# Performance work log

Hardware: AMD Instinct MI355X
Metric: run time of the kernel (lower is better)

## Reference

```python
import jax, jax.numpy as jnp
import numpy as np


def _conv1x1(x, w, b):
    # x: [B,Cin,H,W], w: [Cout,Cin], b: [Cout]
    return jnp.einsum('bchw,oc->bohw', x, w) + b[None, :, None, None]


def setup_inputs() -> dict:
    key = jax.random.key(0)
    ks = jax.random.split(key, 9)
    C, Cb = 256, 128
    B, H, W = 8, 32, 32
    s_in = 1.0 / np.sqrt(C)
    s_bn = 1.0 / np.sqrt(Cb)
    return {
        'x': jax.random.normal(ks[0], (B, C, H, W), dtype=jnp.float32),
        'theta_w': jax.random.uniform(ks[1], (Cb, C), jnp.float32, -s_in, s_in),
        'theta_b': jax.random.uniform(ks[2], (Cb,), jnp.float32, -s_in, s_in),
        'phi_w': jax.random.uniform(ks[3], (Cb, C), jnp.float32, -s_in, s_in),
        'phi_b': jax.random.uniform(ks[4], (Cb,), jnp.float32, -s_in, s_in),
        'g_w': jax.random.uniform(ks[5], (Cb, C), jnp.float32, -s_in, s_in),
        'g_b': jax.random.uniform(ks[6], (Cb,), jnp.float32, -s_in, s_in),
        'W_w': jax.random.uniform(ks[7], (C, Cb), jnp.float32, -s_bn, s_bn),
        'W_b': jax.random.uniform(ks[8], (C,), jnp.float32, -s_bn, s_bn),
    }


def reference(x, theta_w, theta_b, phi_w, phi_b, g_w, g_b, W_w, W_b):
    B, C, H, Wd = x.shape
    Cb = theta_w.shape[0]
    theta = _conv1x1(x, theta_w, theta_b).reshape(-1, Cb)      # [N, Cb] (row-major, as torch)
    phi = _conv1x1(x, phi_w, phi_b).reshape(Cb, -1)            # [Cb, N]
    g = _conv1x1(x, g_w, g_b).reshape(-1, Cb)                  # [N, Cb]
    attn = jax.nn.softmax(theta @ phi, axis=1)                 # [N, N] global attention
    out = (attn @ g).reshape(B, -1, H, Wd)                     # [B, Cb, H, W]
    return _conv1x1(out, W_w, W_b) + x
```

## Files before the change

kernel.cpp:

```cpp
#include <hip/hip_runtime.h>

typedef unsigned short u16;
typedef __attribute__((ext_vector_type(8))) short short8;
typedef __attribute__((ext_vector_type(4))) float f32x4;

__device__ __forceinline__ u16 f2bf(float f){
  union { float f; unsigned u; } v; v.f = f;
  unsigned u = v.u;
  u += 0x7fffu + ((u >> 16) & 1u);
  return (u16)(u >> 16);
}
__device__ __forceinline__ float bf2f(u16 h){
  union { unsigned u; float f; } v; v.u = ((unsigned)h) << 16;
  return v.f;
}

__global__ __launch_bounds__(256) void wcast_kernel(
    const float* __restrict__ tw, const float* __restrict__ pw,
    const float* __restrict__ gw, u16* __restrict__ Wall)
{
  int i = blockIdx.x*256 + threadIdx.x;
  const float* src = (i < 8192) ? tw : (i < 16384) ? pw : gw;
  int off = (i & 8191) * 4;
  float4 v = *(const float4*)(src + off);
  ushort4 o;
  o.x = f2bf(v.x); o.y = f2bf(v.y); o.z = f2bf(v.z); o.w = f2bf(v.w);
  *(ushort4*)(Wall + (size_t)i*4) = o;
}

__global__ __launch_bounds__(256) void xcast_kernel(
    const float* __restrict__ x, u16* __restrict__ XT)
{
  __shared__ float tile[64][69];
  const int b = blockIdx.z, c0 = blockIdx.y*64, hw0 = blockIdx.x*64;
  const int t = threadIdx.x;
  {
    int r = t >> 2, cs = (t & 3) * 16;
    const float* s = x + (size_t)(b*256 + c0 + r)*1024 + hw0 + cs;
    #pragma unroll
    for (int i=0;i<4;i++)
      *(float4*)&tile[r][cs + i*4] = *(const float4*)(s + i*4);
  }
  __syncthreads();
  {
    int hr = t >> 2, cc = (t & 3) * 16;
    __align__(16) u16 tmp[16];
    #pragma unroll
    for (int i=0;i<16;i++) tmp[i] = f2bf(tile[cc + i][hr]);
    u16* d = XT + (size_t)(b*1024 + hw0 + hr)*256 + c0 + cc;
    *(uint4*)d     = *(uint4*)&tmp[0];
    *(uint4*)(d+8) = *(uint4*)&tmp[8];
  }
}

__global__ __launch_bounds__(256, 2) void proj_mfma_kernel(
    const u16* __restrict__ XT, const u16* __restrict__ Wall,
    const float* __restrict__ tb, const float* __restrict__ pb,
    const float* __restrict__ gb,
    u16* __restrict__ T, u16* __restrict__ PHI, u16* __restrict__ G)
{
  __shared__ __align__(16) u16 Ws[128][136];
  __shared__ __align__(16) u16 Xs[128][136];
  const int proj = blockIdx.x, qg = blockIdx.y;
  const int b = qg >> 3, hw0 = (qg & 7) * 128;
  const int q0 = qg * 128;
  const u16* Wsrc = Wall + (size_t)proj * 32768;
  const float* bias = (proj==0) ? tb : (proj==1) ? pb : gb;
  u16* out          = (proj==0) ? T  : (proj==1) ? PHI : G;
  const int t = threadIdx.x;
  const int wave = t >> 6, lane = t & 63;
  const int quad = lane >> 4, n16 = lane & 15;

  f32x4 acc[8][2];
  #pragma unroll
  for (int mt=0;mt<8;mt++)
    #pragma unroll
    for (int nt=0;nt<2;nt++){ f32x4 z = {0.f,0.f,0.f,0.f}; acc[mt][nt] = z; }

  for (int c0 = 0; c0 < 256; c0 += 128){
    __syncthreads();
    {
      int row = t >> 1, cb = (t & 1) * 64;
      const u16* s1 = Wsrc + (size_t)row*256 + c0 + cb;
      #pragma unroll
      for (int i=0;i<8;i++)
        *(uint4*)&Ws[row][cb + i*8] = *(const uint4*)(s1 + i*8);
      const u16* s2 = XT + (size_t)(q0 + row)*256 + c0 + cb;
      #pragma unroll
      for (int i=0;i<8;i++)
        *(uint4*)&Xs[row][cb + i*8] = *(const uint4*)(s2 + i*8);
    }
    __syncthreads();
    #pragma unroll
    for (int kc=0; kc<4; kc++){
      short8 xf[2];
      #pragma unroll
      for (int nt=0;nt<2;nt++)
        xf[nt] = *(const short8*)&Xs[wave*32 + nt*16 + n16][kc*32 + quad*8];
      #pragma unroll
      for (int mt=0;mt<8;mt++){
        short8 wf = *(const short8*)&Ws[mt*16 + n16][kc*32 + quad*8];
        #pragma unroll
        for (int nt=0;nt<2;nt++)
          acc[mt][nt] = __builtin_amdgcn_mfma_f32_16x16x32_bf16(wf, xf[nt], acc[mt][nt], 0, 0, 0);
      }
    }
  }
  #pragma unroll
  for (int mt=0;mt<8;mt++){
    float4 bv = *(const float4*)&bias[mt*16 + quad*4];
    float bb[4] = {bv.x, bv.y, bv.z, bv.w};
    #pragma unroll
    for (int nt=0;nt<2;nt++)
      #pragma unroll
      for (int r=0;r<4;r++)
        out[(size_t)b*131072 + (size_t)(mt*16 + quad*4 + r)*1024
            + hw0 + wave*32 + nt*16 + n16] = f2bf(acc[mt][nt][r] + bb[r]);
  }
}

__global__ __launch_bounds__(256) void transpose_bf_kernel(
    const u16* __restrict__ src, u16* __restrict__ dst, int R, int C)
{
  __shared__ u16 tile[64][72];
  const int t = threadIdx.x;
  const int c0 = blockIdx.x*64, r0 = blockIdx.y*64;
  {
    int rr = t >> 2, cs = (t & 3) * 16;
    const u16* s = src + (size_t)(r0+rr)*C + c0 + cs;
    uint4 a0 = *(const uint4*)s;
    uint4 a1 = *(const uint4*)(s+8);
    *(uint4*)&tile[rr][cs]   = a0;
    *(uint4*)&tile[rr][cs+8] = a1;
  }
  __syncthreads();
  {
    int cc = t >> 2, rs = (t & 3) * 16;
    __align__(16) u16 tmp[16];
    #pragma unroll
    for (int i=0;i<16;i++) tmp[i] = tile[rs+i][cc];
    u16* d = dst + (size_t)(c0+cc)*R + r0 + rs;
    *(uint4*)d     = *(uint4*)&tmp[0];
    *(uint4*)(d+8) = *(uint4*)&tmp[8];
  }
}

__global__ __launch_bounds__(256, 2) void attn_kernel(
    const u16* __restrict__ Tq, const u16* __restrict__ Kk,
    const u16* __restrict__ Vt, u16* __restrict__ Opart,
    float* __restrict__ lpart)
{
  __shared__ __align__(16) u16 Ks[64][136];
  __shared__ __align__(16) u16 Vs[128][72];
  __shared__ __align__(16) u16 Pall[4][4608];

  const int t = threadIdx.x;
  const int wave = t >> 6, lane = t & 63;
  const int quad = lane >> 4, n16 = lane & 15;
  const int s  = blockIdx.x & 15;
  const int qg = blockIdx.x >> 4;
  const int q0 = qg*256 + wave*64;
  u16* Pw = Pall[wave];
  u16*   Os = Opart + (size_t)s * 1048576;
  float* ls = lpart + (size_t)s * 8192;

  short8 qa[4][4];
  #pragma unroll
  for (int mt=0;mt<4;mt++)
    #pragma unroll
    for (int kc=0;kc<4;kc++)
      qa[mt][kc] = *(const short8*)(Tq + (size_t)(q0 + mt*16 + n16)*128 + kc*32 + quad*8);

  f32x4 o[4][8];
  float lp[4];
  #pragma unroll
  for (int mt=0;mt<4;mt++){
    #pragma unroll
    for (int dt=0;dt<8;dt++){ f32x4 z = {0.f,0.f,0.f,0.f}; o[mt][dt] = z; }
    lp[mt] = 0.f;
  }

  const int krow = t >> 2, kcs = (t & 3) * 32;
  const int vrow = t >> 1, vcs = (t & 1) * 32;
  const int wmask = n16 & 14;

  for (int kt = s*8; kt < s*8 + 8; kt++){
    const int key0 = kt * 64;
    __syncthreads();
    #pragma unroll
    for (int i=0;i<4;i++)
      *(uint4*)&Ks[krow][kcs + i*8] =
        *(const uint4*)(Kk + (size_t)(key0 + krow)*128 + kcs + i*8);
    #pragma unroll
    for (int i=0;i<4;i++)
      *(uint4*)&Vs[vrow][vcs + i*8] =
        *(const uint4*)(Vt + (size_t)vrow*8192 + key0 + vcs + i*8);
    __syncthreads();

    #pragma unroll
    for (int ntk=0; ntk<4; ntk++){
      short8 kf[4];
      #pragma unroll
      for (int kc=0;kc<4;kc++)
        kf[kc] = *(const short8*)&Ks[ntk*16 + n16][kc*32 + quad*8];
      #pragma unroll
      for (int mtq=0;mtq<4;mtq++){
        f32x4 sa = {0.f,0.f,0.f,0.f};
        #pragma unroll
        for (int kc=0;kc<4;kc++)
          sa = __builtin_amdgcn_mfma_f32_16x16x32_bf16(kf[kc], qa[mtq][kc], sa, 0, 0, 0);
        u16 pb[4];
        #pragma unroll
        for (int r=0;r<4;r++){
          float pe = exp2f(sa[r] * 1.4426950408889634f);
          lp[mtq] += pe;
          pb[r] = f2bf(pe);
        }
        uint2 pk;
        pk.x = ((unsigned)pb[1] << 16) | pb[0];
        pk.y = ((unsigned)pb[3] << 16) | pb[2];
        *(uint2*)(Pw + (mtq*16 + n16)*72 + (((ntk*4 + quad) ^ wmask) << 2)) = pk;
      }
    }

    __builtin_amdgcn_s_waitcnt(0xC07F);

    #pragma unroll
    for (int kb=0; kb<2; kb++){
      short8 pf[4];
      #pragma unroll
      for (int mtq=0;mtq<4;mtq++)
        pf[mtq] = *(const short8*)(Pw + (mtq*16 + n16)*72 + (((kb*8 + quad*2) ^ wmask) << 2));
      #pragma unroll
      for (int dt=0; dt<8; dt++){
        short8 vfd = *(const short8*)&Vs[dt*16 + n16][kb*32 + quad*8];
        #pragma unroll
        for (int mtq=0;mtq<4;mtq++)
          o[mtq][dt] = __builtin_amdgcn_mfma_f32_16x16x32_bf16(pf[mtq], vfd, o[mtq][dt], 0, 0, 0);
      }
    }
  }

  float l[4];
  #pragma unroll
  for (int mt=0;mt<4;mt++){
    float v = lp[mt];
    v += __shfl_xor(v, 16, 64);
    v += __shfl_xor(v, 32, 64);
    l[mt] = v;
  }

  #pragma unroll
  for (int mt=0;mt<4;mt++){
    #pragma unroll
    for (int r=0;r<4;r++){
      __align__(16) u16 tmp[8];
      #pragma unroll
      for (int dt=0;dt<8;dt++) tmp[dt] = f2bf(o[mt][dt][r]);
      *(uint4*)(Os + (size_t)(q0 + mt*16 + quad*4 + r)*128 + n16*8) = *(uint4*)tmp;
    }
    if (lane < 16)
      ls[q0 + mt*16 + lane] = l[mt];
  }
}

__global__ __launch_bounds__(256) void merge_o_kernel(
    const u16* __restrict__ Opart, const float* __restrict__ lpart, int S,
    u16* __restrict__ OmT)
{
  __shared__ u16 Tm[64][136];
  __shared__ float lrow[64];
  const int t = threadIdx.x;
  const int row0 = blockIdx.x * 64;
  const int b  = row0 >> 10;
  const int j0 = (row0 >> 3) & 127;

  if (t < 64){
    float v = 0.f;
    for (int sp=0; sp<S; sp++) v += lpart[sp*8192 + row0 + t];
    lrow[t] = 1.0f / v;
  }

  const int rl = t >> 2;
  const int cb = (t & 3) * 32;
  float acc[32];
  #pragma unroll
  for (int j=0;j<32;j++) acc[j] = 0.f;
  for (int sp=0; sp<S; sp++){
    const u16* p = Opart + (size_t)sp*1048576 + (size_t)(row0 + rl)*128 + cb;
    #pragma unroll
    for (int q=0;q<4;q++){
      ushort4 v = *(const ushort4*)(p + q*8);
      ushort4 w = *(const ushort4*)(p + q*8 + 4);
      acc[q*8+0] += bf2f(v.x); acc[q*8+1] += bf2f(v.y);
      acc[q*8+2] += bf2f(v.z); acc[q*8+3] += bf2f(v.w);
      acc[q*8+4] += bf2f(w.x); acc[q*8+5] += bf2f(w.y);
      acc[q*8+6] += bf2f(w.z); acc[q*8+7] += bf2f(w.w);
    }
  }
  __syncthreads();
  const float inv = lrow[rl];
  #pragma unroll
  for (int j=0;j<32;j++){
    int cp = cb + j;
    int ch = (cp & 7)*16 + (cp >> 3);
    Tm[rl][ch] = f2bf(acc[j] * inv);
  }
  __syncthreads();
  {
    const int hwhi = t >> 5;
    const int chb  = (t & 31) * 4;
    #pragma unroll
    for (int c=0;c<4;c++){
      int ch = chb + c;
      __align__(16) u16 tmp[8];
      #pragma unroll
      for (int jl=0;jl<8;jl++) tmp[jl] = Tm[jl*8 + hwhi][ch];
      *(uint4*)(OmT + (size_t)(b*1024 + hwhi*128 + ch)*128 + j0) = *(uint4*)tmp;
    }
  }
}

__global__ __launch_bounds__(256, 2) void final_mfma_kernel(
    const float* __restrict__ Ww, const float* __restrict__ Wb,
    const u16* __restrict__ OmT, const float* __restrict__ x,
    float* __restrict__ outp)
{
  __shared__ __align__(16) u16 Ws[64][136];
  __shared__ __align__(16) u16 Os[128][136];
  const int co0 = blockIdx.x * 64, qg = blockIdx.y;
  const int b = qg >> 3, hw0 = (qg & 7) * 128;
  const int q0 = qg * 128;
  const int t = threadIdx.x;
  const int wave = t >> 6, lane = t & 63;
  const int quad = lane >> 4, n16 = lane & 15;

  {
    int row = t >> 2, cbf = (t & 3) * 32;
    const float* sw = Ww + (size_t)(co0 + row)*128 + cbf;
    #pragma unroll
    for (int i=0;i<8;i++){
      float4 v = *(const float4*)(sw + i*4);
      u16* d = &Ws[row][cbf + i*4];
      d[0]=f2bf(v.x); d[1]=f2bf(v.y); d[2]=f2bf(v.z); d[3]=f2bf(v.w);
    }
  }
  {
    int row = t >> 1, cb = (t & 1) * 64;
    const u16* so = OmT + (size_t)(q0 + row)*128 + cb;
    #pragma unroll
    for (int i=0;i<8;i++)
      *(uint4*)&Os[row][cb + i*8] = *(const uint4*)(so + i*8);
  }
  __syncthreads();

  f32x4 acc[4][2];
  #pragma unroll
  for (int mt=0;mt<4;mt++)
    #pragma unroll
    for (int nt=0;nt<2;nt++){ f32x4 z = {0.f,0.f,0.f,0.f}; acc[mt][nt] = z; }

  #pragma unroll
  for (int kc=0; kc<4; kc++){
    short8 xf[2];
    #pragma unroll
    for (int nt=0;nt<2;nt++)
      xf[nt] = *(const short8*)&Os[wave*32 + nt*16 + n16][kc*32 + quad*8];
    #pragma unroll
    for (int mt=0;mt<4;mt++){
      short8 wf = *(const short8*)&Ws[mt*16 + n16][kc*32 + quad*8];
      #pragma unroll
      for (int nt=0;nt<2;nt++)
        acc[mt][nt] = __builtin_amdgcn_mfma_f32_16x16x32_bf16(wf, xf[nt], acc[mt][nt], 0, 0, 0);
    }
  }

  #pragma unroll
  for (int mt=0;mt<4;mt++){
    float4 bv = *(const float4*)&Wb[co0 + mt*16 + quad*4];
    float bb[4] = {bv.x, bv.y, bv.z, bv.w};
    #pragma unroll
    for (int nt=0;nt<2;nt++)
      #pragma unroll
      for (int r=0;r<4;r++){
        size_t idx = (size_t)b*262144 + (size_t)(co0 + mt*16 + quad*4 + r)*1024
                   + hw0 + wave*32 + nt*16 + n16;
        outp[idx] = acc[mt][nt][r] + bb[r] + x[idx];
      }
  }
}

extern "C" void kernel_launch(void* const* d_in, const int* in_sizes, int n_in,
                              void* d_out, int out_size, void* d_ws, size_t ws_size,
                              hipStream_t stream)
{
  (void)in_sizes; (void)n_in; (void)out_size; (void)ws_size;
  const float* x  = (const float*)d_in[0];
  const float* tw = (const float*)d_in[1];
  const float* tb = (const float*)d_in[2];
  const float* pw = (const float*)d_in[3];
  const float* pb = (const float*)d_in[4];
  const float* gw = (const float*)d_in[5];
  const float* gb = (const float*)d_in[6];
  const float* Ww = (const float*)d_in[7];
  const float* Wb = (const float*)d_in[8];
  float* outp = (float*)d_out;

  char* ws = (char*)d_ws;
  const size_t MB = 1u << 20;
  u16*   Tbf   = (u16*)(ws);
  u16*   PHIbf = (u16*)(ws + 2*MB);
  u16*   Gbf   = (u16*)(ws + 4*MB);
  u16*   Kbf   = (u16*)(ws + 6*MB);
  u16*   VTbf  = (u16*)(ws + 8*MB);
  u16*   Opart = (u16*)(ws + 10*MB);
  u16*   XT    = (u16*)(ws + 10*MB);
  u16*   Wall  = (u16*)(ws + 14*MB);
  float* lpart = (float*)(ws + 2*MB);
  u16*   OmT   = (u16*)(ws + 4*MB);

  wcast_kernel<<<dim3(96), 256, 0, stream>>>(tw, pw, gw, Wall);
  xcast_kernel<<<dim3(16, 4, 8), 256, 0, stream>>>(x, XT);
  proj_mfma_kernel<<<dim3(3, 64), 256, 0, stream>>>(XT, Wall, tb, pb, gb,
                                                    Tbf, PHIbf, Gbf);
  transpose_bf_kernel<<<dim3(128, 2), 256, 0, stream>>>(PHIbf, Kbf, 128, 8192);
  transpose_bf_kernel<<<dim3(2, 128), 256, 0, stream>>>(Gbf, VTbf, 8192, 128);
  attn_kernel<<<dim3(512), 256, 0, stream>>>(Tbf, Kbf, VTbf, Opart, lpart);
  merge_o_kernel<<<dim3(128), 256, 0, stream>>>(Opart, lpart, 16, OmT);
  final_mfma_kernel<<<dim3(4, 64), 256, 0, stream>>>(Ww, Wb, OmT, x, outp);
}
```

Before: 189.0 us.

## Fuse casts, projections and PHI transpose into one kernel; prefetch K/V tiles

Result: slower. 236.6 us (+25.2%).

```diff
diff --git a/kernel.cpp b/kernel.cpp
--- a/kernel.cpp
+++ b/kernel.cpp
@@ -15,107 +15,110 @@
   return v.f;
 }
 
-__global__ __launch_bounds__(256) void wcast_kernel(
-    const float* __restrict__ tw, const float* __restrict__ pw,
-    const float* __restrict__ gw, u16* __restrict__ Wall)
-{
-  int i = blockIdx.x*256 + threadIdx.x;
-  const float* src = (i < 8192) ? tw : (i < 16384) ? pw : gw;
-  int off = (i & 8191) * 4;
-  float4 v = *(const float4*)(src + off);
-  ushort4 o;
-  o.x = f2bf(v.x); o.y = f2bf(v.y); o.z = f2bf(v.z); o.w = f2bf(v.w);
-  *(ushort4*)(Wall + (size_t)i*4) = o;
-}
-
-__global__ __launch_bounds__(256) void xcast_kernel(
-    const float* __restrict__ x, u16* __restrict__ XT)
-{
-  __shared__ float tile[64][69];
-  const int b = blockIdx.z, c0 = blockIdx.y*64, hw0 = blockIdx.x*64;
-  const int t = threadIdx.x;
-  {
-    int r = t >> 2, cs = (t & 3) * 16;
-    const float* s = x + (size_t)(b*256 + c0 + r)*1024 + hw0 + cs;
-    #pragma unroll
-    for (int i=0;i<4;i++)
-      *(float4*)&tile[r][cs + i*4] = *(const float4*)(s + i*4);
-  }
-  __syncthreads();
-  {
-    int hr = t >> 2, cc = (t & 3) * 16;
-    __align__(16) u16 tmp[16];
-    #pragma unroll
-    for (int i=0;i<16;i++) tmp[i] = f2bf(tile[cc + i][hr]);
-    u16* d = XT + (size_t)(b*1024 + hw0 + hr)*256 + c0 + cc;
-    *(uint4*)d     = *(uint4*)&tmp[0];
-    *(uint4*)(d+8) = *(uint4*)&tmp[8];
-  }
-}
-
-__global__ __launch_bounds__(256, 2) void proj_mfma_kernel(
-    const u16* __restrict__ XT, const u16* __restrict__ Wall,
-    const float* __restrict__ tb, const float* __restrict__ pb,
-    const float* __restrict__ gb,
-    u16* __restrict__ T, u16* __restrict__ PHI, u16* __restrict__ G)
+__global__ __launch_bounds__(256, 2) void megaproj_kernel(
+    const float* __restrict__ x,
+    const float* __restrict__ tw, const float* __restrict__ tb,
+    const float* __restrict__ pw, const float* __restrict__ pb,
+    const float* __restrict__ gw, const float* __restrict__ gb,
+    u16* __restrict__ Tq, u16* __restrict__ Kk, u16* __restrict__ Gn)
 {
   __shared__ __align__(16) u16 Ws[128][136];
-  __shared__ __align__(16) u16 Xs[128][136];
-  const int proj = blockIdx.x, qg = blockIdx.y;
-  const int b = qg >> 3, hw0 = (qg & 7) * 128;
-  const int q0 = qg * 128;
-  const u16* Wsrc = Wall + (size_t)proj * 32768;
-  const float* bias = (proj==0) ? tb : (proj==1) ? pb : gb;
-  u16* out          = (proj==0) ? T  : (proj==1) ? PHI : G;
+  __shared__ __align__(16) u16 Ls[128][136];
+  const int qg = blockIdx.x;
+  const int b = qg >> 3, hwhi = qg & 7, hw0 = hwhi * 128;
   const int t = threadIdx.x;
   const int wave = t >> 6, lane = t & 63;
   const int quad = lane >> 4, n16 = lane & 15;
 
-  f32x4 acc[8][2];
-  #pragma unroll
-  for (int mt=0;mt<8;mt++)
-    #pragma unroll
-    for (int nt=0;nt<2;nt++){ f32x4 z = {0.f,0.f,0.f,0.f}; acc[mt][nt] = z; }
-
-  for (int c0 = 0; c0 < 256; c0 += 128){
+  short8 xf[8][2];
+  #pragma unroll
+  for (int kc=0;kc<8;kc++)
+    #pragma unroll
+    for (int nt=0;nt<2;nt++){
+      const int q = wave*32 + nt*16 + n16;
+      const float* xs = x + ((size_t)b*256 + kc*32 + quad*8)*1024 + hw0 + q;
+      __align__(16) u16 tmp[8];
+      #pragma unroll
+      for (int j=0;j<8;j++) tmp[j] = f2bf(xs[(size_t)j*1024]);
+      xf[kc][nt] = *(short8*)tmp;
+    }
+
+  for (int proj=0; proj<3; proj++){
+    const float* W    = (proj==0) ? tw : (proj==1) ? pw : gw;
+    const float* bias = (proj==0) ? tb : (proj==1) ? pb : gb;
+
+    f32x4 acc[8][2];
+    #pragma unroll
+    for (int mt=0;mt<8;mt++)
+      #pragma unroll
+      for (int nt=0;nt<2;nt++){ f32x4 z = {0.f,0.f,0.f,0.f}; acc[mt][nt] = z; }
+
+    for (int half=0; half<2; half++){
+      __syncthreads();
+      {
+        int row = t >> 1, seg = (t & 1) * 64;
+        const float* sw = W + (size_t)row*256 + half*128 + seg;
+        #pragma unroll
+        for (int i=0;i<8;i++){
+          float4 a = *(const float4*)(sw + i*8);
+          float4 c = *(const float4*)(sw + i*8 + 4);
+          __align__(16) u16 t8[8];
+          t8[0]=f2bf(a.x); t8[1]=f2bf(a.y); t8[2]=f2bf(a.z); t8[3]=f2bf(a.w);
+          t8[4]=f2bf(c.x); t8[5]=f2bf(c.y); t8[6]=f2bf(c.z); t8[7]=f2bf(c.w);
+          *(uint4*)&Ws[row][seg + i*8] = *(uint4*)t8;
+        }
+      }
+      __syncthreads();
+      #pragma unroll
+      for (int kc4=0; kc4<4; kc4++){
+        #pragma unroll
+        for (int mt=0;mt<8;mt++){
+          short8 wf = *(const short8*)&Ws[mt*16 + n16][kc4*32 + quad*8];
+          #pragma unroll
+          for (int nt=0;nt<2;nt++)
+            acc[mt][nt] = __builtin_amdgcn_mfma_f32_16x16x32_bf16(
+                            wf, xf[half*4+kc4][nt], acc[mt][nt], 0, 0, 0);
+        }
+      }
+    }
+
+    #pragma unroll
+    for (int mt=0;mt<8;mt++){
+      float4 bv = *(const float4*)&bias[mt*16 + quad*4];
+      float bb[4] = {bv.x, bv.y, bv.z, bv.w};
+      #pragma unroll
+      for (int nt=0;nt<2;nt++){
+        const int q = wave*32 + nt*16 + n16;
+        #pragma unroll
+        for (int r=0;r<4;r++){
+          const int co = mt*16 + quad*4 + r;
+          u16 v = f2bf(acc[mt][nt][r] + bb[r]);
+          if (proj == 1) Ls[q][((co & 7) << 4) | (co >> 3)] = v;
+          else           Ls[co][q] = v;
+        }
+      }
+    }
     __syncthreads();
-    {
-      int row = t >> 1, cb = (t & 1) * 64;
-      const u16* s1 = Wsrc + (size_t)row*256 + c0 + cb;
+
+    if (proj == 1){
+      #pragma unroll
+      for (int pi=0; pi<4; pi++){
+        int p = t*4 + pi;
+        int colow = p >> 7, hwlo = p & 127;
+        uint4 v0 = *(const uint4*)&Ls[hwlo][colow*16];
+        uint4 v1 = *(const uint4*)&Ls[hwlo][colow*16 + 8];
+        u16* d = Kk + (size_t)(colow*1024 + hw0 + hwlo)*128 + b*16;
+        *(uint4*)d     = v0;
+        *(uint4*)(d+8) = v1;
+      }
+    } else {
+      u16* out = (proj==0) ? Tq : Gn;
+      int row = t >> 1, seg = (t & 1) * 64;
+      u16* d = out + (size_t)(b*1024 + row*8 + hwhi)*128 + seg;
       #pragma unroll
       for (int i=0;i<8;i++)
-        *(uint4*)&Ws[row][cb + i*8] = *(const uint4*)(s1 + i*8);
-      const u16* s2 = XT + (size_t)(q0 + row)*256 + c0 + cb;
-      #pragma unroll
-      for (int i=0;i<8;i++)
-        *(uint4*)&Xs[row][cb + i*8] = *(const uint4*)(s2 + i*8);
-    }
-    __syncthreads();
-    #pragma unroll
-    for (int kc=0; kc<4; kc++){
-      short8 xf[2];
-      #pragma unroll
-      for (int nt=0;nt<2;nt++)
-        xf[nt] = *(const short8*)&Xs[wave*32 + nt*16 + n16][kc*32 + quad*8];
-      #pragma unroll
-      for (int mt=0;mt<8;mt++){
-        short8 wf = *(const short8*)&Ws[mt*16 + n16][kc*32 + quad*8];
-        #pragma unroll
-        for (int nt=0;nt<2;nt++)
-          acc[mt][nt] = __builtin_amdgcn_mfma_f32_16x16x32_bf16(wf, xf[nt], acc[mt][nt], 0, 0, 0);
-      }
-    }
-  }
-  #pragma unroll
-  for (int mt=0;mt<8;mt++){
-    float4 bv = *(const float4*)&bias[mt*16 + quad*4];
-    float bb[4] = {bv.x, bv.y, bv.z, bv.w};
-    #pragma unroll
-    for (int nt=0;nt<2;nt++)
-      #pragma unroll
-      for (int r=0;r<4;r++)
-        out[(size_t)b*131072 + (size_t)(mt*16 + quad*4 + r)*1024
-            + hw0 + wave*32 + nt*16 + n16] = f2bf(acc[mt][nt][r] + bb[r]);
+        *(uint4*)(d + i*8) = *(const uint4*)&Ls[row][seg + i*8];
+    }
   }
 }
 
@@ -184,18 +187,33 @@
   const int vrow = t >> 1, vcs = (t & 1) * 32;
   const int wmask = n16 & 14;
 
+  uint4 kreg[4], vreg[4];
+  {
+    const int key0 = s*8*64;
+    #pragma unroll
+    for (int i=0;i<4;i++)
+      kreg[i] = *(const uint4*)(Kk + (size_t)(key0 + krow)*128 + kcs + i*8);
+    #pragma unroll
+    for (int i=0;i<4;i++)
+      vreg[i] = *(const uint4*)(Vt + (size_t)vrow*8192 + key0 + vcs + i*8);
+  }
+
   for (int kt = s*8; kt < s*8 + 8; kt++){
-    const int key0 = kt * 64;
     __syncthreads();
     #pragma unroll
-    for (int i=0;i<4;i++)
-      *(uint4*)&Ks[krow][kcs + i*8] =
-        *(const uint4*)(Kk + (size_t)(key0 + krow)*128 + kcs + i*8);
-    #pragma unroll
-    for (int i=0;i<4;i++)
-      *(uint4*)&Vs[vrow][vcs + i*8] =
-        *(const uint4*)(Vt + (size_t)vrow*8192 + key0 + vcs + i*8);
+    for (int i=0;i<4;i++) *(uint4*)&Ks[krow][kcs + i*8] = kreg[i];
+    #pragma unroll
+    for (int i=0;i<4;i++) *(uint4*)&Vs[vrow][vcs + i*8] = vreg[i];
     __syncthreads();
+    if (kt + 1 < s*8 + 8){
+      const int key0 = (kt+1)*64;
+      #pragma unroll
+      for (int i=0;i<4;i++)
+        kreg[i] = *(const uint4*)(Kk + (size_t)(key0 + krow)*128 + kcs + i*8);
+      #pragma unroll
+      for (int i=0;i<4;i++)
+        vreg[i] = *(const uint4*)(Vt + (size_t)vrow*8192 + key0 + vcs + i*8);
+    }
 
     #pragma unroll
     for (int ntk=0; ntk<4; ntk++){
@@ -409,21 +427,15 @@
   char* ws = (char*)d_ws;
   const size_t MB = 1u << 20;
   u16*   Tbf   = (u16*)(ws);
-  u16*   PHIbf = (u16*)(ws + 2*MB);
+  float* lpart = (float*)(ws + 2*MB);
   u16*   Gbf   = (u16*)(ws + 4*MB);
   u16*   Kbf   = (u16*)(ws + 6*MB);
   u16*   VTbf  = (u16*)(ws + 8*MB);
   u16*   Opart = (u16*)(ws + 10*MB);
-  u16*   XT    = (u16*)(ws + 10*MB);
-  u16*   Wall  = (u16*)(ws + 14*MB);
-  float* lpart = (float*)(ws + 2*MB);
   u16*   OmT   = (u16*)(ws + 4*MB);
 
-  wcast_kernel<<<dim3(96), 256, 0, stream>>>(tw, pw, gw, Wall);
-  xcast_kernel<<<dim3(16, 4, 8), 256, 0, stream>>>(x, XT);
-  proj_mfma_kernel<<<dim3(3, 64), 256, 0, stream>>>(XT, Wall, tb, pb, gb,
-                                                    Tbf, PHIbf, Gbf);
-  transpose_bf_kernel<<<dim3(128, 2), 256, 0, stream>>>(PHIbf, Kbf, 128, 8192);
+  megaproj_kernel<<<dim3(64), 256, 0, stream>>>(x, tw, tb, pw, pb, gw, gb,
+                                                Tbf, Kbf, Gbf);
   transpose_bf_kernel<<<dim3(2, 128), 256, 0, stream>>>(Gbf, VTbf, 8192, 128);
   attn_kernel<<<dim3(512), 256, 0, stream>>>(Tbf, Kbf, VTbf, Opart, lpart);
   merge_o_kernel<<<dim3(128), 256, 0, stream>>>(Opart, lpart, 16, OmT);
```
